# Kernel tuning notes

Measured on AMD Instinct MI355X. Metric: run time of the kernel, lower is better.

Reference implementation:

```python
import jax, jax.numpy as jnp
import numpy as np

TAU = 2.0          # spikingjelly LIFNode default
V_RESET = 0.0      # hard reset target
V_TH = 1.0         # v_threshold init kwarg
SG_ALPHA = 4.0     # sigmoid surrogate alpha

@jax.custom_vjp
def heaviside(x):
    return (x >= 0.0).astype(x.dtype)

def _heaviside_fwd(x):
    return heaviside(x), x

def _heaviside_bwd(x, g):
    s = jax.nn.sigmoid(SG_ALPHA * x)
    return (g * SG_ALPHA * s * (1.0 - s),)

heaviside.defvjp(_heaviside_fwd, _heaviside_bwd)

def setup_inputs() -> dict:
    key = jax.random.key(0)
    ks = jax.random.split(key, 6)
    T, B, I, H = 512, 64, 512, 512
    sI, sH = 1.0 / np.sqrt(I), 1.0 / np.sqrt(H)
    return {
        "input": jax.random.normal(ks[0], (T, B, I), jnp.float32),
        "hidden": jax.random.normal(ks[1], (T, B, H), jnp.float32),
        "W_ih": jax.random.normal(ks[2], (H, I), jnp.float32) * sI,
        "b_ih": jax.random.normal(ks[3], (H,), jnp.float32) * sI,
        "W_hh": jax.random.normal(ks[4], (H, H), jnp.float32) * sH,
        "b_hh": jax.random.normal(ks[5], (H,), jnp.float32) * sH,
    }

def reference(input, hidden, W_ih, b_ih, W_hh, b_hh):
    # multi-step linears: [T,B,I]@[I,H] + [T,B,H]@[H,H]
    x = (jnp.einsum('tbi,hi->tbh', input, W_ih) + b_ih
         + jnp.einsum('tbj,hj->tbh', hidden, W_hh) + b_hh)  # [T,B,H]

    T, B, H = x.shape
    v0 = jnp.zeros((B, H), x.dtype)

    def step(v, xt):
        # decay_input=True: v += (x - (v - v_reset)) / tau
        v = v + (xt - (v - V_RESET)) / TAU
        spike = heaviside(v - V_TH)
        v = (1.0 - spike) * v + spike * V_RESET  # hard reset
        return v, spike

    _, spikes = jax.lax.scan(step, v0, x)  # spikes: [T,B,H]
    return spikes
```

## Files before the change

kernel.cpp:

```cpp
#include <hip/hip_runtime.h>


constexpr int Mtot = 32768;
constexpr int Ntot = 512;
constexpr int Kd   = 512;
constexpr int BM = 128, BN = 64, BK = 32;

__device__ __forceinline__ int swz(int row, int k) {
    int sw = ((row >> 3) ^ row) & 7;
    int c  = (k >> 2) ^ sw;
    return row * BK + (c << 2) + (k & 3);
}

__device__ __forceinline__ void do_phase(
    const float* __restrict__ Ap, const float* __restrict__ Wp,
    float (&acc)[8][4], float* As, float* Ws,
    int m0, int n0, int tid, int tm, int tn)
{
    for (int k0 = 0; k0 < Kd; k0 += BK) {
        __syncthreads();
#pragma unroll
        for (int q = 0; q < 4; ++q) {
            int lin = q * 256 + tid;
            int row = lin >> 3, ch = lin & 7;
            float4 v4 = *(const float4*)(Ap + (size_t)(m0 + row) * Kd + k0 + ch * 4);
            *(float4*)(As + swz(row, ch * 4)) = v4;
        }
#pragma unroll
        for (int q = 0; q < 2; ++q) {
            int lin = q * 256 + tid;
            int row = lin >> 3, ch = lin & 7;
            float4 v4 = *(const float4*)(Wp + (size_t)(n0 + row) * Kd + k0 + ch * 4);
            *(float4*)(Ws + swz(row, ch * 4)) = v4;
        }
        __syncthreads();
#pragma unroll
        for (int k4 = 0; k4 < BK; k4 += 4) {
            float4 a[8], w[4];
#pragma unroll
            for (int i = 0; i < 8; ++i)
                a[i] = *(const float4*)(As + swz(tm * 8 + i, k4));
#pragma unroll
            for (int j = 0; j < 4; ++j)
                w[j] = *(const float4*)(Ws + swz(tn * 4 + j, k4));
#pragma unroll
            for (int i = 0; i < 8; ++i) {
#pragma unroll
                for (int j = 0; j < 4; ++j) {
                    acc[i][j] = fmaf(a[i].x, w[j].x, acc[i][j]);
                    acc[i][j] = fmaf(a[i].y, w[j].y, acc[i][j]);
                    acc[i][j] = fmaf(a[i].z, w[j].z, acc[i][j]);
                    acc[i][j] = fmaf(a[i].w, w[j].w, acc[i][j]);
                }
            }
        }
    }
}

__global__ __launch_bounds__(256, 2) void gemm_x(
    const float* __restrict__ A1, const float* __restrict__ A2,
    const float* __restrict__ W1, const float* __restrict__ bi,
    const float* __restrict__ W2, const float* __restrict__ bh,
    float* __restrict__ out)
{
    __shared__ float As[BM * BK];
    __shared__ float Ws[BN * BK];

    const int tid = threadIdx.x;
    const int bm = blockIdx.x >> 3;
    const int bn = blockIdx.x & 7;
    const int m0 = bm * BM, n0 = bn * BN;
    const int tm = tid >> 4, tn = tid & 15;

    float acc1[8][4];
    float acc2[8][4];
#pragma unroll
    for (int i = 0; i < 8; ++i)
#pragma unroll
        for (int j = 0; j < 4; ++j) { acc1[i][j] = 0.f; acc2[i][j] = 0.f; }

    do_phase(A1, W1, acc1, As, Ws, m0, n0, tid, tm, tn);
    do_phase(A2, W2, acc2, As, Ws, m0, n0, tid, tm, tn);

    const float4 bi4 = *(const float4*)(bi + n0 + tn * 4);
    const float4 bh4 = *(const float4*)(bh + n0 + tn * 4);
#pragma unroll
    for (int i = 0; i < 8; ++i) {
        float4 o;
        o.x = ((acc1[i][0] + bi4.x) + acc2[i][0]) + bh4.x;
        o.y = ((acc1[i][1] + bi4.y) + acc2[i][1]) + bh4.y;
        o.z = ((acc1[i][2] + bi4.z) + acc2[i][2]) + bh4.z;
        o.w = ((acc1[i][3] + bi4.w) + acc2[i][3]) + bh4.w;
        *(float4*)(out + (size_t)(m0 + tm * 8 + i) * Ntot + n0 + tn * 4) = o;
    }
}

__global__ __launch_bounds__(256) void lif_scan(float* __restrict__ x)
{
    const int tid = blockIdx.x * blockDim.x + threadIdx.x;
    float v = 0.f;
    for (int tb = 0; tb < 512; tb += 8) {
        float xv[8];
#pragma unroll
        for (int u = 0; u < 8; ++u)
            xv[u] = x[(tb + u) * 32768 + tid];
#pragma unroll
        for (int u = 0; u < 8; ++u) {
            v = v + (xv[u] - v) * 0.5f;
            float s = (v - 1.0f >= 0.0f) ? 1.0f : 0.0f;
            x[(tb + u) * 32768 + tid] = s;
            v = (1.0f - s) * v;
        }
    }
}

extern "C" void kernel_launch(void* const* d_in, const int* in_sizes, int n_in,
                              void* d_out, int out_size, void* d_ws, size_t ws_size,
                              hipStream_t stream) {
    const float* input  = (const float*)d_in[0];
    const float* hidden = (const float*)d_in[1];
    const float* W_ih   = (const float*)d_in[2];
    const float* b_ih   = (const float*)d_in[3];
    const float* W_hh   = (const float*)d_in[4];
    const float* b_hh   = (const float*)d_in[5];
    float* out = (float*)d_out;

    dim3 grid((Mtot / BM) * (Ntot / BN));
    dim3 block(256);
    gemm_x<<<grid, block, 0, stream>>>(input, hidden, W_ih, b_ih, W_hh, b_hh, out);
    lif_scan<<<128, 256, 0, stream>>>(out);
}
```

Baseline: 550.1 us.

## Register-prefetch GEMM tiles, remap block order, new swizzle, deeper scan unroll

The GEMM now prefetches the next K-tile from global memory into registers while the current tile is being computed, so load latency overlaps the FMAs. It also changes the shared-memory swizzle, remaps block indices so consecutive blocks share the same N tile, and raises launch_bounds occupancy to 3 blocks per CU. The LIF scan loads 16 timesteps per batch instead of 8. These changes cost extra registers, which may spill under the tighter occupancy bound.

New measurement: 763.4 us. 38.8% more time.

```diff
diff --git a/kernel.cpp b/kernel.cpp
--- a/kernel.cpp
+++ b/kernel.cpp
@@ -2,88 +2,99 @@
 
 
 constexpr int Mtot = 32768;
-constexpr int Ntot = 512;
-constexpr int Kd   = 512;
-constexpr int BM = 128, BN = 64, BK = 32;
 
-__device__ __forceinline__ int swz(int row, int k) {
-    int sw = ((row >> 3) ^ row) & 7;
-    int c  = (k >> 2) ^ sw;
-    return row * BK + (c << 2) + (k & 3);
-}
 
-__device__ __forceinline__ void do_phase(
-    const float* __restrict__ Ap, const float* __restrict__ Wp,
-    float (&acc)[8][4], float* As, float* Ws,
-    int m0, int n0, int tid, int tm, int tn)
-{
-    for (int k0 = 0; k0 < Kd; k0 += BK) {
-        __syncthreads();
-#pragma unroll
-        for (int q = 0; q < 4; ++q) {
-            int lin = q * 256 + tid;
-            int row = lin >> 3, ch = lin & 7;
-            float4 v4 = *(const float4*)(Ap + (size_t)(m0 + row) * Kd + k0 + ch * 4);
-            *(float4*)(As + swz(row, ch * 4)) = v4;
-        }
-#pragma unroll
-        for (int q = 0; q < 2; ++q) {
-            int lin = q * 256 + tid;
-            int row = lin >> 3, ch = lin & 7;
-            float4 v4 = *(const float4*)(Wp + (size_t)(n0 + row) * Kd + k0 + ch * 4);
-            *(float4*)(Ws + swz(row, ch * 4)) = v4;
-        }
-        __syncthreads();
-#pragma unroll
-        for (int k4 = 0; k4 < BK; k4 += 4) {
-            float4 a[8], w[4];
-#pragma unroll
-            for (int i = 0; i < 8; ++i)
-                a[i] = *(const float4*)(As + swz(tm * 8 + i, k4));
-#pragma unroll
-            for (int j = 0; j < 4; ++j)
-                w[j] = *(const float4*)(Ws + swz(tn * 4 + j, k4));
-#pragma unroll
-            for (int i = 0; i < 8; ++i) {
-#pragma unroll
-                for (int j = 0; j < 4; ++j) {
-                    acc[i][j] = fmaf(a[i].x, w[j].x, acc[i][j]);
-                    acc[i][j] = fmaf(a[i].y, w[j].y, acc[i][j]);
-                    acc[i][j] = fmaf(a[i].z, w[j].z, acc[i][j]);
-                    acc[i][j] = fmaf(a[i].w, w[j].w, acc[i][j]);
-                }
-            }
-        }
+#define STAGE_STORE()                                                         \
+    _Pragma("unroll") for (int q = 0; q < 4; ++q) *(float4*)(As + awr[q]) = ar[q]; \
+    _Pragma("unroll") for (int q = 0; q < 2; ++q) *(float4*)(Ws + wwr[q]) = wr[q];
+
+#define STAGE_LOAD(AP, WP)                                                    \
+    _Pragma("unroll") for (int q = 0; q < 4; ++q) ar[q] = *(const float4*)((AP) + aoff[q]); \
+    _Pragma("unroll") for (int q = 0; q < 2; ++q) wr[q] = *(const float4*)((WP) + woff[q]);
+
+#define FMA_PHASE(ACC)                                                        \
+    _Pragma("unroll")                                                         \
+    for (int kc = 0; kc < 8; ++kc) {                                          \
+        float4 w4[4];                                                         \
+        _Pragma("unroll")                                                     \
+        for (int j = 0; j < 4; ++j)                                           \
+            w4[j] = *(const float4*)((const char*)Ws + tn * 512 + j * 128 + (((kc ^ tn) & 7) << 4)); \
+        _Pragma("unroll")                                                     \
+        for (int i = 0; i < 8; ++i) {                                         \
+            float4 a4 = *(const float4*)((const char*)As + (tm * 8 + i) * 128 + ((kc ^ i) << 4)); \
+            _Pragma("unroll")                                                 \
+            for (int j = 0; j < 4; ++j) {                                     \
+                ACC[i][j] = fmaf(a4.x, w4[j].x, ACC[i][j]);                   \
+                ACC[i][j] = fmaf(a4.y, w4[j].y, ACC[i][j]);                   \
+                ACC[i][j] = fmaf(a4.z, w4[j].z, ACC[i][j]);                   \
+                ACC[i][j] = fmaf(a4.w, w4[j].w, ACC[i][j]);                   \
+            }                                                                 \
+        }                                                                     \
     }
-}
 
-__global__ __launch_bounds__(256, 2) void gemm_x(
-    const float* __restrict__ A1, const float* __restrict__ A2,
-    const float* __restrict__ W1, const float* __restrict__ bi,
-    const float* __restrict__ W2, const float* __restrict__ bh,
+__global__ __launch_bounds__(256, 3) void gemm_x(
+    const float* __restrict__ input, const float* __restrict__ hidden,
+    const float* __restrict__ W_ih, const float* __restrict__ b_ih,
+    const float* __restrict__ W_hh, const float* __restrict__ b_hh,
     float* __restrict__ out)
 {
-    __shared__ float As[BM * BK];
-    __shared__ float Ws[BN * BK];
+    __shared__ __align__(16) float As[128 * 32];
+    __shared__ __align__(16) float Ws[64 * 32];
 
     const int tid = threadIdx.x;
-    const int bm = blockIdx.x >> 3;
-    const int bn = blockIdx.x & 7;
-    const int m0 = bm * BM, n0 = bn * BN;
+    const int tile = ((blockIdx.x & 7) << 8) | (blockIdx.x >> 3);
+    const int bm = tile >> 3, bn = tile & 7;
+    const int m0 = bm * 128, n0 = bn * 64;
     const int tm = tid >> 4, tn = tid & 15;
 
-    float acc1[8][4];
-    float acc2[8][4];
+    int aoff[4], awr[4], woff[2], wwr[2];
+#pragma unroll
+    for (int q = 0; q < 4; ++q) {
+        int lin = q * 256 + tid, row = lin >> 3, s4 = lin & 7;
+        aoff[q] = (m0 + row) * 512 + s4 * 4;
+        awr[q]  = row * 32 + ((s4 ^ (row & 7)) << 2);
+    }
+#pragma unroll
+    for (int q = 0; q < 2; ++q) {
+        int lin = q * 256 + tid, row = lin >> 3, s4 = lin & 7;
+        woff[q] = (n0 + row) * 512 + s4 * 4;
+        wwr[q]  = row * 32 + ((s4 ^ ((row >> 2) & 7)) << 2);
+    }
+
+    float acc1[8][4], acc2[8][4];
 #pragma unroll
     for (int i = 0; i < 8; ++i)
 #pragma unroll
         for (int j = 0; j < 4; ++j) { acc1[i][j] = 0.f; acc2[i][j] = 0.f; }
 
-    do_phase(A1, W1, acc1, As, Ws, m0, n0, tid, tm, tn);
-    do_phase(A2, W2, acc2, As, Ws, m0, n0, tid, tm, tn);
+    float4 ar[4], wr[2];
+    STAGE_LOAD(input, W_ih);
 
-    const float4 bi4 = *(const float4*)(bi + n0 + tn * 4);
-    const float4 bh4 = *(const float4*)(bh + n0 + tn * 4);
+#pragma unroll 1
+    for (int kt = 0; kt < 16; ++kt) {
+        STAGE_STORE();
+        __syncthreads();
+        const float* An = (kt < 15) ? (input + (kt + 1) * 32) : hidden;
+        const float* Wn = (kt < 15) ? (W_ih + (kt + 1) * 32) : W_hh;
+        STAGE_LOAD(An, Wn);
+        FMA_PHASE(acc1);
+        __syncthreads();
+    }
+#pragma unroll 1
+    for (int kt = 0; kt < 16; ++kt) {
+        STAGE_STORE();
+        __syncthreads();
+        if (kt < 15) {
+            const float* An = hidden + (kt + 1) * 32;
+            const float* Wn = W_hh + (kt + 1) * 32;
+            STAGE_LOAD(An, Wn);
+        }
+        FMA_PHASE(acc2);
+        __syncthreads();
+    }
+
+    const float4 bi4 = *(const float4*)(b_ih + n0 + tn * 4);
+    const float4 bh4 = *(const float4*)(b_hh + n0 + tn * 4);
 #pragma unroll
     for (int i = 0; i < 8; ++i) {
         float4 o;
@@ -91,7 +102,7 @@
         o.y = ((acc1[i][1] + bi4.y) + acc2[i][1]) + bh4.y;
         o.z = ((acc1[i][2] + bi4.z) + acc2[i][2]) + bh4.z;
         o.w = ((acc1[i][3] + bi4.w) + acc2[i][3]) + bh4.w;
-        *(float4*)(out + (size_t)(m0 + tm * 8 + i) * Ntot + n0 + tn * 4) = o;
+        *(float4*)(out + (size_t)(m0 + tm * 8 + i) * 512 + n0 + tn * 4) = o;
     }
 }
 
@@ -99,13 +110,13 @@
 {
     const int tid = blockIdx.x * blockDim.x + threadIdx.x;
     float v = 0.f;
-    for (int tb = 0; tb < 512; tb += 8) {
-        float xv[8];
+    for (int tb = 0; tb < 512; tb += 16) {
+        float xv[16];
 #pragma unroll
-        for (int u = 0; u < 8; ++u)
+        for (int u = 0; u < 16; ++u)
             xv[u] = x[(tb + u) * 32768 + tid];
 #pragma unroll
-        for (int u = 0; u < 8; ++u) {
+        for (int u = 0; u < 16; ++u) {
             v = v + (xv[u] - v) * 0.5f;
             float s = (v - 1.0f >= 0.0f) ? 1.0f : 0.0f;
             x[(tb + u) * 32768 + tid] = s;
@@ -125,8 +136,7 @@
     const float* b_hh   = (const float*)d_in[5];
     float* out = (float*)d_out;
 
-    dim3 grid((Mtot / BM) * (Ntot / BN));
-    dim3 block(256);
-    gemm_x<<<grid, block, 0, stream>>>(input, hidden, W_ih, b_ih, W_hh, b_hh, out);
-    lif_scan<<<128, 256, 0, stream>>>(out);
+    gemm_x<<<dim3(2048), dim3(256), 0, stream>>>(
+        input, hidden, W_ih, b_ih, W_hh, b_hh, out);
+    lif_scan<<<dim3(128), dim3(256), 0, stream>>>(out);
 }
```
